# Optimization experiments

Hardware: AMD Instinct MI355X
Metric: run time of the kernel (lower is better)

Reference implementation:

```python
import jax, jax.numpy as jnp
import numpy as np

N = 4096
INPLANES = 256
PLANES = 256
LOC_PLANES = 256


def _ln(x, g, b, eps=1e-5):
    m = jnp.mean(x, axis=-1, keepdims=True)
    v = jnp.mean(jnp.square(x - m), axis=-1, keepdims=True)
    return (x - m) * jax.lax.rsqrt(v + eps) * g + b


def setup_inputs() -> dict:
    key = jax.random.key(0)
    ks = jax.random.split(key, 12)
    s = 0.02
    cat_dim = INPLANES + LOC_PLANES
    return {
        "img_fea": jax.random.normal(ks[0], (N, INPLANES), jnp.float32),
        "loc_fea": jax.random.normal(ks[1], (N, LOC_PLANES), jnp.float32),
        # conv11: Basic1d(cat_dim -> inplanes, bias=True) + ReLU
        "w11": jax.random.normal(ks[2], (cat_dim, INPLANES), jnp.float32) * s,
        "b11": jnp.zeros((INPLANES,), jnp.float32),
        # conv12: Linear(inplanes -> inplanes)
        "w12": jax.random.normal(ks[3], (INPLANES, INPLANES), jnp.float32) * s,
        "b12": jnp.zeros((INPLANES,), jnp.float32),
        # conv21: Basic1d(cat_dim -> inplanes, bias=True) + ReLU
        "w21": jax.random.normal(ks[4], (cat_dim, INPLANES), jnp.float32) * s,
        "b21": jnp.zeros((INPLANES,), jnp.float32),
        # conv22: Linear(inplanes -> inplanes*planes) -- hypernetwork weight generator
        "w22": jax.random.normal(ks[5], (INPLANES, INPLANES * PLANES), jnp.float32) * s,
        "b22": jnp.zeros((INPLANES * PLANES,), jnp.float32),
        # br: LayerNorm(planes)
        "lnbr_g": jnp.ones((PLANES,), jnp.float32),
        "lnbr_b": jnp.zeros((PLANES,), jnp.float32),
        # conv3: Basic1d(planes -> planes, bias=False) -> Linear + LayerNorm + ReLU
        "w3": jax.random.normal(ks[6], (PLANES, PLANES), jnp.float32) * s,
        "ln3_g": jnp.ones((PLANES,), jnp.float32),
        "ln3_b": jnp.zeros((PLANES,), jnp.float32),
    }


def reference(img_fea, loc_fea, w11, b11, w12, b12, w21, b21, w22, b22,
              lnbr_g, lnbr_b, w3, ln3_g, ln3_b):
    cat = jnp.concatenate([img_fea, loc_fea], axis=1)          # [N, 512]
    h11 = jax.nn.relu(cat @ w11 + b11)                          # [N, 256]
    wgt12 = h11 @ w12 + b12                                     # [N, 256]
    h21 = jax.nn.relu(cat @ w21 + b21)                          # [N, 256]
    wgt22 = (h21 @ w22 + b22).reshape(-1, INPLANES, PLANES)     # [N, 256, 256]
    out = jnp.einsum('bi,bio->bo', wgt12, wgt22)                # batched GEMV
    out = jax.nn.relu(_ln(out, lnbr_g, lnbr_b))
    out = jax.nn.relu(_ln(out @ w3, ln3_g, ln3_b))
    return (out, loc_fea)
```

## Files before the change

### kernel.cpp

```cpp
#include <hip/hip_runtime.h>
#include <stdint.h>

typedef unsigned short u16;
typedef __bf16 bf16;
typedef bf16 bf16x8 __attribute__((ext_vector_type(8)));
typedef u16 u16x8 __attribute__((ext_vector_type(8)));
typedef float f32x4 __attribute__((ext_vector_type(4)));

__device__ __forceinline__ u16 f2bf(float f) {
  union { float f; unsigned u; } v; v.f = f;
  unsigned u = v.u;
  u += 0x7FFFu + ((u >> 16) & 1u);
  return (u16)(u >> 16);
}

__device__ __forceinline__ bf16x8 as_bf16x8(u16x8 v) {
  return __builtin_bit_cast(bf16x8, v);
}

__device__ __forceinline__ f32x4 mfma16(bf16x8 a, bf16x8 b, f32x4 c) {
  return __builtin_amdgcn_mfma_f32_16x16x32_bf16(a, b, c, 0, 0, 0);
}

#define AS1 __attribute__((address_space(1)))
#define AS3 __attribute__((address_space(3)))
__device__ __forceinline__ void gl_lds16(const u16* g, u16* l) {
  __builtin_amdgcn_global_load_lds((const AS1 void*)g, (AS3 void*)l, 16, 0, 0);
}

__device__ __forceinline__ long wfrag(int b, int i) {
  const int bt = b >> 7, bg = (b >> 6) & 1, nf = (b >> 4) & 3, l15 = b & 15;
  const int ih = (i >> 7) & 1, s4 = (i >> 6) & 1, ks = (i >> 5) & 1;
  const int lhi = (i >> 3) & 3, e = i & 7;
  return ((((((((long)bt * 2 + ih) * 2 + bg) * 2 + s4) * 2 + ks) * 4 + lhi) * 4
            + nf) * 16 + l15) * 8 + e;
}

__global__ __launch_bounds__(256) void k_transpose(const float* __restrict__ src,
    u16* __restrict__ dst, long dstStride, long dstOff) {
  __shared__ float tile[64][65];
  const int t = threadIdx.x;
  const int tr = t >> 6, tc = t & 63;
  const long rb = (long)blockIdx.x * 64;
  const int ob = blockIdx.y * 64;
#pragma unroll
  for (int i = 0; i < 16; ++i) {
    int r = i * 4 + tr;
    tile[r][tc] = src[(rb + r) * 256 + ob + tc];
  }
  __syncthreads();
  const int orow = t >> 2, seg = t & 3;
#pragma unroll
  for (int h = 0; h < 2; ++h) {
    u16x8 v;
#pragma unroll
    for (int j = 0; j < 8; ++j) v[j] = f2bf(tile[seg * 16 + h * 8 + j][orow]);
    *(u16x8*)&dst[(long)(ob + orow) * dstStride + dstOff + rb + seg * 16 + h * 8] = v;
  }
}

__global__ __launch_bounds__(256) void k_transpose_multi(
    const float* __restrict__ b22, const float* __restrict__ w11,
    const float* __restrict__ w21, const float* __restrict__ w12,
    const float* __restrict__ w3, u16* __restrict__ W2T, u16* __restrict__ W11T,
    u16* __restrict__ W21T, u16* __restrict__ W12T, u16* __restrict__ W3T) {
  __shared__ float tile[64][65];
  const int x = blockIdx.x;
  const float* src; u16* dst; long stride, off; int rb;
  if (x < 4)       { src = b22; dst = W2T;  stride = 65792; off = 65536; rb = x; }
  else if (x < 12) { src = w11; dst = W11T; stride = 512;   off = 0;     rb = x - 4; }
  else if (x < 20) { src = w21; dst = W21T; stride = 512;   off = 0;     rb = x - 12; }
  else if (x < 24) { src = w12; dst = W12T; stride = 256;   off = 0;     rb = x - 20; }
  else             { src = w3;  dst = W3T;  stride = 256;   off = 0;     rb = x - 24; }
  const long rbase = (long)rb * 64;
  const int t = threadIdx.x;
  const int tr = t >> 6, tc = t & 63;
  const int ob = blockIdx.y * 64;
#pragma unroll
  for (int i = 0; i < 16; ++i) {
    int r = i * 4 + tr;
    tile[r][tc] = src[(rbase + r) * 256 + ob + tc];
  }
  __syncthreads();
  const int orow = t >> 2, seg = t & 3;
#pragma unroll
  for (int h = 0; h < 2; ++h) {
    u16x8 v;
#pragma unroll
    for (int j = 0; j < 8; ++j) v[j] = f2bf(tile[seg * 16 + h * 8 + j][orow]);
    *(u16x8*)&dst[(long)(ob + orow) * stride + off + rbase + seg * 16 + h * 8] = v;
  }
}

__device__ __forceinline__ void gemm_small_core(const float* A0, const float* A1,
    int K, const u16* WT, f32x4 (&acc)[4], int o0, long row) {
  const int lane = threadIdx.x & 63;
  const int l15 = lane & 15, lhi = lane >> 4;
  const int kg = lhi * 8;
  for (int ks = 0; ks < K; ks += 32) {
    int k = ks + kg;
    const float* ap = (A1 != nullptr && k >= 256) ? (A1 + row * 256 + (k - 256))
                                                  : (A0 + row * 256 + k);
    f32x4 f0 = *(const f32x4*)ap;
    f32x4 f1 = *(const f32x4*)(ap + 4);
    u16x8 a;
    a[0]=f2bf(f0[0]); a[1]=f2bf(f0[1]); a[2]=f2bf(f0[2]); a[3]=f2bf(f0[3]);
    a[4]=f2bf(f1[0]); a[5]=f2bf(f1[1]); a[6]=f2bf(f1[2]); a[7]=f2bf(f1[3]);
    bf16x8 av = as_bf16x8(a);
#pragma unroll
    for (int nf = 0; nf < 4; ++nf) {
      int o = o0 + nf * 16 + l15;
      u16x8 braw = *(const u16x8*)(WT + (long)o * K + k);
      acc[nf] = mfma16(av, as_bf16x8(braw), acc[nf]);
    }
  }
}

__global__ __launch_bounds__(256) void k_gemm_h21(const float* __restrict__ img,
    const float* __restrict__ loc, const u16* __restrict__ W21T,
    const float* __restrict__ b21, float* __restrict__ h21) {
  const int t = threadIdx.x;
  const int wid = t >> 6, lane = t & 63;
  const int l15 = lane & 15, lhi = lane >> 4;
  const int b0 = blockIdx.x * 16;
  const int o0 = wid * 64;
  const long row = b0 + l15;
  f32x4 acc[4] = {};
  gemm_small_core(img, loc, 512, W21T, acc, o0, row);
#pragma unroll
  for (int nf = 0; nf < 4; ++nf) {
    int o = o0 + nf * 16 + l15;
    float bs = b21[o];
#pragma unroll
    for (int r = 0; r < 4; ++r) {
      long b = b0 + lhi * 4 + r;
      h21[b * 256 + o] = fmaxf(acc[nf][r] + bs, 0.f);
    }
  }
}

__global__ __launch_bounds__(256) void k_fuse12(const float* __restrict__ img,
    const float* __restrict__ loc, const u16* __restrict__ W11T,
    const float* __restrict__ b11, const u16* __restrict__ W12T,
    const float* __restrict__ b12, u16* __restrict__ wgt12F) {
  __shared__ u16 A16[16][264];
  const int t = threadIdx.x;
  const int wid = t >> 6, lane = t & 63;
  const int l15 = lane & 15, lhi = lane >> 4;
  const int b0 = blockIdx.x * 16;
  const int o0 = wid * 64;
  const long row = b0 + l15;
  f32x4 a1[4] = {};
  gemm_small_core(img, loc, 512, W11T, a1, o0, row);
#pragma unroll
  for (int nf = 0; nf < 4; ++nf) {
    int o = o0 + nf * 16 + l15;
    float bs = b11[o];
#pragma unroll
    for (int r = 0; r < 4; ++r)
      A16[lhi * 4 + r][o] = f2bf(fmaxf(a1[nf][r] + bs, 0.f));
  }
  __syncthreads();
  f32x4 a2[4] = {};
  for (int ks = 0; ks < 256; ks += 32) {
    const int k = ks + lhi * 8;
    bf16x8 av = as_bf16x8(*(const u16x8*)&A16[l15][k]);
#pragma unroll
    for (int nf = 0; nf < 4; ++nf) {
      int o = o0 + nf * 16 + l15;
      u16x8 braw = *(const u16x8*)(W12T + (long)o * 256 + k);
      a2[nf] = mfma16(av, as_bf16x8(braw), a2[nf]);
    }
  }
#pragma unroll
  for (int nf = 0; nf < 4; ++nf) {
    const int i = o0 + nf * 16 + l15;
    const float bs = b12[i];
#pragma unroll
    for (int r = 0; r < 4; ++r) {
      const int b = b0 + lhi * 4 + r;
      wgt12F[wfrag(b, i)] = f2bf(a2[nf][r] + bs);
    }
  }
}

__global__ __launch_bounds__(256, 2) void k_big(const u16* __restrict__ W2T,
    const float* __restrict__ h21, const u16* __restrict__ wgt12F,
    float* __restrict__ partials) {
  __shared__ u16 ldsWh[16384];
  __shared__ u16 ldsA[2][8192];
  const int t = threadIdx.x;
  const int wid = t >> 6, lane = t & 63;
  const int l15 = lane & 15, lhi = lane >> 4;
  const int n = blockIdx.x;
  const int chunk = n & 7;
  const int q = n >> 3;
  const int o_base = (q & 1) * 128;
  const int bt = q >> 1;
  const int b0 = bt * 128;
  const int og = wid >> 1, bg = wid & 1;
  const int nkb = (chunk == 7) ? 33 : 32;
  const int NSh = nkb * 2;

  const int ar = t >> 1;
  const int ah = t & 1;
  const u16* agbase = W2T + (long)(o_base + ar) * 65792 + chunk * 8192 + ah * 32;

  f32x4 acc[4][4] = {};
  u16x8 sa[4];

  auto LOADA = [&](int poff) {
    const u16* p = agbase + poff;
#pragma unroll
    for (int j = 0; j < 4; ++j) sa[j] = *(const u16x8*)(p + j * 8);
  };
  auto WRITEA = [&](int buf) {
#pragma unroll
    for (int j = 0; j < 4; ++j) {
      const int sg = ah * 4 + j;
      *(u16x8*)&ldsA[buf][ar * 64 + ((sg ^ (ar & 7)) * 8)] = sa[j];
    }
  };

  const int bvb = (bg * 2048 + lhi * 128 + l15 * 2) * 4;

#pragma unroll 1
  for (int ih = 0; ih < 2; ++ih) {
    {
      const u16* wsrc = wgt12F + ((long)(bt * 2 + ih)) * 16384 + lane * 8;
#pragma unroll
      for (int j = 0; j < 8; ++j)
        gl_lds16(wsrc + (wid * 8 + j) * 512, &ldsWh[(wid * 8 + j) * 512]);
    }
    LOADA(ih * 128);
    WRITEA(0);
    __syncthreads();

    int s = 0;
#pragma unroll 1
    for (int kb = 0; kb < nkb; ++kb) {
      const int kk = chunk * 32 + kb;
      float sc[4];
#pragma unroll
      for (int nf = 0; nf < 4; ++nf)
        sc[nf] = (kk < 256)
                   ? h21[(long)(b0 + bg * 64 + nf * 16 + l15) * 256 + kk]
                   : 1.0f;
      f32x4 sub[4][4] = {};
#pragma unroll
      for (int s4 = 0; s4 < 2; ++s4) {
        const int buf = s & 1;
        const bool last = (s + 1 >= NSh);
        if (!last)
          LOADA(s4 == 0 ? kb * 256 + ih * 128 + 64 : (kb + 1) * 256 + ih * 128);
#pragma unroll
        for (int ks = 0; ks < 2; ++ks) {
          const int x = ks * 4 + lhi;
          bf16x8 af[4], bv[4];
#pragma unroll
          for (int mf = 0; mf < 4; ++mf) {
            const int ro = og * 64 + mf * 16 + l15;
            af[mf] = as_bf16x8(
                *(const u16x8*)&ldsA[buf][ro * 64 + ((x ^ (ro & 7)) * 8)]);
          }
          const int bvo = bvb + (s4 * 2 + ks) * 2048;
#pragma unroll
          for (int nf = 0; nf < 4; ++nf)
            bv[nf] = as_bf16x8(*(const u16x8*)&ldsWh[bvo + nf * 128]);
          __builtin_amdgcn_s_setprio(1);
#pragma unroll
          for (int mf = 0; mf < 4; ++mf)
#pragma unroll
            for (int nf = 0; nf < 4; ++nf)
              sub[mf][nf] = mfma16(af[mf], bv[nf], sub[mf][nf]);
          __builtin_amdgcn_s_setprio(0);
        }
        if (!last) WRITEA(buf ^ 1);
        __syncthreads();
        ++s;
      }
#pragma unroll
      for (int mf = 0; mf < 4; ++mf)
#pragma unroll
        for (int nf = 0; nf < 4; ++nf)
          acc[mf][nf] += sc[nf] * sub[mf][nf];
    }
  }

  const long cb = (long)chunk * (256L * 4096);
#pragma unroll
  for (int mf = 0; mf < 4; ++mf)
#pragma unroll
    for (int nf = 0; nf < 4; ++nf)
#pragma unroll
      for (int r = 0; r < 4; ++r) {
        const int o = o_base + og * 64 + mf * 16 + lhi * 4 + r;
        const int bgl = b0 + bg * 64 + nf * 16 + l15;
        partials[cb + (long)o * 4096 + bgl] = acc[mf][nf][r];
      }
}

__global__ __launch_bounds__(256) void k_tail(const float* __restrict__ parts,
    const float* __restrict__ lng, const float* __restrict__ lnb,
    const u16* __restrict__ W3T, const float* __restrict__ g3,
    const float* __restrict__ bb3, float* __restrict__ out) {
  __shared__ float tile[16][260];
  __shared__ u16 A16[16][264];
  __shared__ float s1s[4][16], s2s[4][16];
  __shared__ float mz[16], rz[16];
  const int t = threadIdx.x;
  const int b0 = blockIdx.x * 16;
  {
    const int oq = t >> 2, bseg = t & 3;
#pragma unroll
    for (int j = 0; j < 4; ++j) {
      const int o = oq + j * 64;
      f32x4 s = {};
#pragma unroll
      for (int c = 0; c < 8; ++c)
        s += *(const f32x4*)&parts[(long)c * (256L * 4096) + (long)o * 4096 + b0 + bseg * 4];
#pragma unroll
      for (int q = 0; q < 4; ++q) tile[bseg * 4 + q][o] = s[q];
    }
  }
  __syncthreads();
  {
    const int r = t >> 4, og = t & 15;
    float v[16];
    float s1 = 0.f, s2 = 0.f;
#pragma unroll
    for (int q = 0; q < 16; ++q) {
      float x = tile[r][og * 16 + q];
      v[q] = x; s1 += x; s2 += x * x;
    }
    s1 += __shfl_xor(s1, 1); s2 += __shfl_xor(s2, 1);
    s1 += __shfl_xor(s1, 2); s2 += __shfl_xor(s2, 2);
    s1 += __shfl_xor(s1, 4); s2 += __shfl_xor(s2, 4);
    s1 += __shfl_xor(s1, 8); s2 += __shfl_xor(s2, 8);
    float mean = s1 * (1.f / 256.f);
    float var = s2 * (1.f / 256.f) - mean * mean;
    float rstd = rsqrtf(var + 1e-5f);
    u16x8 w0, w1;
#pragma unroll
    for (int q = 0; q < 16; ++q) {
      int o = og * 16 + q;
      float x = (v[q] - mean) * rstd * lng[o] + lnb[o];
      x = fmaxf(x, 0.f);
      if (q < 8) w0[q] = f2bf(x); else w1[q - 8] = f2bf(x);
    }
    *(u16x8*)&A16[r][og * 16] = w0;
    *(u16x8*)&A16[r][og * 16 + 8] = w1;
  }
  __syncthreads();
  const int wid = t >> 6, lane = t & 63;
  const int l15 = lane & 15, lhi = lane >> 4;
  const int wo = wid * 64;
  f32x4 acc[4] = {};
  for (int ks = 0; ks < 256; ks += 32) {
    const int k = ks + lhi * 8;
    bf16x8 av = as_bf16x8(*(const u16x8*)&A16[l15][k]);
#pragma unroll
    for (int nf = 0; nf < 4; ++nf) {
      int o = wo + nf * 16 + l15;
      u16x8 braw = *(const u16x8*)(W3T + (long)o * 256 + k);
      acc[nf] = mfma16(av, as_bf16x8(braw), acc[nf]);
    }
  }
#pragma unroll
  for (int r = 0; r < 4; ++r) {
    float s1 = 0.f, s2 = 0.f;
#pragma unroll
    for (int nf = 0; nf < 4; ++nf) { float x = acc[nf][r]; s1 += x; s2 += x * x; }
    s1 += __shfl_xor(s1, 1); s2 += __shfl_xor(s2, 1);
    s1 += __shfl_xor(s1, 2); s2 += __shfl_xor(s2, 2);
    s1 += __shfl_xor(s1, 4); s2 += __shfl_xor(s2, 4);
    s1 += __shfl_xor(s1, 8); s2 += __shfl_xor(s2, 8);
    if (l15 == 0) { s1s[wid][lhi * 4 + r] = s1; s2s[wid][lhi * 4 + r] = s2; }
  }
  __syncthreads();
  if (t < 16) {
    float s1 = s1s[0][t] + s1s[1][t] + s1s[2][t] + s1s[3][t];
    float s2 = s2s[0][t] + s2s[1][t] + s2s[2][t] + s2s[3][t];
    float mean = s1 * (1.f / 256.f);
    float var = s2 * (1.f / 256.f) - mean * mean;
    mz[t] = mean; rz[t] = rsqrtf(var + 1e-5f);
  }
  __syncthreads();
#pragma unroll
  for (int r = 0; r < 4; ++r) {
    const int b = lhi * 4 + r;
    const float mean = mz[b], rstd = rz[b];
#pragma unroll
    for (int nf = 0; nf < 4; ++nf) {
      int o = wo + nf * 16 + l15;
      float x = (acc[nf][r] - mean) * rstd * g3[o] + bb3[o];
      out[(long)(b0 + b) * 256 + o] = fmaxf(x, 0.f);
    }
  }
}

extern "C" void kernel_launch(void* const* d_in, const int* in_sizes, int n_in,
                              void* d_out, int out_size, void* d_ws, size_t ws_size,
                              hipStream_t stream) {
  const float* img = (const float*)d_in[0];
  const float* loc = (const float*)d_in[1];
  const float* w11 = (const float*)d_in[2];
  const float* b11 = (const float*)d_in[3];
  const float* w12 = (const float*)d_in[4];
  const float* b12 = (const float*)d_in[5];
  const float* w21 = (const float*)d_in[6];
  const float* b21 = (const float*)d_in[7];
  const float* w22 = (const float*)d_in[8];
  const float* b22 = (const float*)d_in[9];
  const float* lng = (const float*)d_in[10];
  const float* lnb = (const float*)d_in[11];
  const float* w3  = (const float*)d_in[12];
  const float* g3  = (const float*)d_in[13];
  const float* bb3 = (const float*)d_in[14];

  char* ws = (char*)d_ws;
  u16* W2T    = (u16*)(ws);
  u16* W11T   = (u16*)(ws + 33685504);
  u16* W21T   = (u16*)(ws + 33947648);
  u16* W12T   = (u16*)(ws + 34209792);
  u16* W3T    = (u16*)(ws + 34340864);
  float* h21  = (float*)(ws + 38666240);
  u16* wgt12F = (u16*)(ws + 42860544);
  float* parts = (float*)(ws + 47054848);
  float* outp  = (float*)d_out;

  hipMemcpyAsync(outp + 1048576, loc, 4194304, hipMemcpyDeviceToDevice, stream);

  hipLaunchKernelGGL(k_transpose, dim3(1024, 4), dim3(256), 0, stream,
                     w22, W2T, (long)65792, (long)0);
  hipLaunchKernelGGL(k_transpose_multi, dim3(28, 4), dim3(256), 0, stream,
                     b22, w11, w21, w12, w3, W2T, W11T, W21T, W12T, W3T);

  hipLaunchKernelGGL(k_gemm_h21, dim3(256), dim3(256), 0, stream,
                     img, loc, W21T, b21, h21);
  hipLaunchKernelGGL(k_fuse12, dim3(256), dim3(256), 0, stream,
                     img, loc, W11T, b11, W12T, b12, wgt12F);

  hipLaunchKernelGGL(k_big, dim3(512), dim3(256), 0, stream,
                     W2T, h21, wgt12F, parts);

  hipLaunchKernelGGL(k_tail, dim3(256), dim3(256), 0, stream,
                     parts, lng, lnb, W3T, g3, bb3, outp);
}
```

Measured before the change: 326.8 us.

## Merge transpose and front GEMM launches; deepen global-to-LDS prefetch in main kernel

Folds the two weight transpose kernels into one launch and the h21 GEMM and fused conv11/conv12 kernel into one two-slice grid. This cuts launch overhead and lets independent blocks share the GPU. In the main batched kernel the A-tile register staging becomes two alternating register sets, so global loads are issued two stages ahead and the LDS write happens before compute. The aim is to hide global latency better, at the cost of more registers. The bvb offset is also re-expressed in different units.

```diff
diff --git a/kernel.cpp b/kernel.cpp
--- a/kernel.cpp
+++ b/kernel.cpp
@@ -36,43 +36,25 @@
             + nf) * 16 + l15) * 8 + e;
 }
 
-__global__ __launch_bounds__(256) void k_transpose(const float* __restrict__ src,
-    u16* __restrict__ dst, long dstStride, long dstOff) {
-  __shared__ float tile[64][65];
-  const int t = threadIdx.x;
-  const int tr = t >> 6, tc = t & 63;
-  const long rb = (long)blockIdx.x * 64;
-  const int ob = blockIdx.y * 64;
-#pragma unroll
-  for (int i = 0; i < 16; ++i) {
-    int r = i * 4 + tr;
-    tile[r][tc] = src[(rb + r) * 256 + ob + tc];
-  }
-  __syncthreads();
-  const int orow = t >> 2, seg = t & 3;
-#pragma unroll
-  for (int h = 0; h < 2; ++h) {
-    u16x8 v;
-#pragma unroll
-    for (int j = 0; j < 8; ++j) v[j] = f2bf(tile[seg * 16 + h * 8 + j][orow]);
-    *(u16x8*)&dst[(long)(ob + orow) * dstStride + dstOff + rb + seg * 16 + h * 8] = v;
-  }
-}
-
-__global__ __launch_bounds__(256) void k_transpose_multi(
-    const float* __restrict__ b22, const float* __restrict__ w11,
-    const float* __restrict__ w21, const float* __restrict__ w12,
-    const float* __restrict__ w3, u16* __restrict__ W2T, u16* __restrict__ W11T,
-    u16* __restrict__ W21T, u16* __restrict__ W12T, u16* __restrict__ W3T) {
+__global__ __launch_bounds__(256) void k_transpose_all(
+    const float* __restrict__ w22, const float* __restrict__ b22,
+    const float* __restrict__ w11, const float* __restrict__ w21,
+    const float* __restrict__ w12, const float* __restrict__ w3,
+    u16* __restrict__ W2T, u16* __restrict__ W11T, u16* __restrict__ W21T,
+    u16* __restrict__ W12T, u16* __restrict__ W3T) {
   __shared__ float tile[64][65];
   const int x = blockIdx.x;
-  const float* src; u16* dst; long stride, off; int rb;
-  if (x < 4)       { src = b22; dst = W2T;  stride = 65792; off = 65536; rb = x; }
-  else if (x < 12) { src = w11; dst = W11T; stride = 512;   off = 0;     rb = x - 4; }
-  else if (x < 20) { src = w21; dst = W21T; stride = 512;   off = 0;     rb = x - 12; }
-  else if (x < 24) { src = w12; dst = W12T; stride = 256;   off = 0;     rb = x - 20; }
-  else             { src = w3;  dst = W3T;  stride = 256;   off = 0;     rb = x - 24; }
-  const long rbase = (long)rb * 64;
+  const float* src; u16* dst; long stride, off; long rbase;
+  if (x < 1024)     { src = w22; dst = W2T;  stride = 65792; off = 0;
+                      rbase = (long)x * 64; }
+  else {
+    const int x2 = x - 1024;
+    if (x2 < 4)       { src = b22; dst = W2T;  stride = 65792; off = 65536; rbase = (long)x2 * 64; }
+    else if (x2 < 12) { src = w11; dst = W11T; stride = 512;   off = 0;     rbase = (long)(x2 - 4) * 64; }
+    else if (x2 < 20) { src = w21; dst = W21T; stride = 512;   off = 0;     rbase = (long)(x2 - 12) * 64; }
+    else if (x2 < 24) { src = w12; dst = W12T; stride = 256;   off = 0;     rbase = (long)(x2 - 20) * 64; }
+    else              { src = w3;  dst = W3T;  stride = 256;   off = 0;     rbase = (long)(x2 - 24) * 64; }
+  }
   const int t = threadIdx.x;
   const int tr = t >> 6, tc = t & 63;
   const int ob = blockIdx.y * 64;
@@ -116,33 +98,12 @@
   }
 }
 
-__global__ __launch_bounds__(256) void k_gemm_h21(const float* __restrict__ img,
-    const float* __restrict__ loc, const u16* __restrict__ W21T,
-    const float* __restrict__ b21, float* __restrict__ h21) {
-  const int t = threadIdx.x;
-  const int wid = t >> 6, lane = t & 63;
-  const int l15 = lane & 15, lhi = lane >> 4;
-  const int b0 = blockIdx.x * 16;
-  const int o0 = wid * 64;
-  const long row = b0 + l15;
-  f32x4 acc[4] = {};
-  gemm_small_core(img, loc, 512, W21T, acc, o0, row);
-#pragma unroll
-  for (int nf = 0; nf < 4; ++nf) {
-    int o = o0 + nf * 16 + l15;
-    float bs = b21[o];
-#pragma unroll
-    for (int r = 0; r < 4; ++r) {
-      long b = b0 + lhi * 4 + r;
-      h21[b * 256 + o] = fmaxf(acc[nf][r] + bs, 0.f);
-    }
-  }
-}
-
-__global__ __launch_bounds__(256) void k_fuse12(const float* __restrict__ img,
+__global__ __launch_bounds__(256) void k_front(const float* __restrict__ img,
     const float* __restrict__ loc, const u16* __restrict__ W11T,
     const float* __restrict__ b11, const u16* __restrict__ W12T,
-    const float* __restrict__ b12, u16* __restrict__ wgt12F) {
+    const float* __restrict__ b12, u16* __restrict__ wgt12F,
+    const u16* __restrict__ W21T, const float* __restrict__ b21,
+    float* __restrict__ h21) {
   __shared__ u16 A16[16][264];
   const int t = threadIdx.x;
   const int wid = t >> 6, lane = t & 63;
@@ -150,6 +111,21 @@
   const int b0 = blockIdx.x * 16;
   const int o0 = wid * 64;
   const long row = b0 + l15;
+  if (blockIdx.y == 1) {
+    f32x4 acc[4] = {};
+    gemm_small_core(img, loc, 512, W21T, acc, o0, row);
+#pragma unroll
+    for (int nf = 0; nf < 4; ++nf) {
+      int o = o0 + nf * 16 + l15;
+      float bs = b21[o];
+#pragma unroll
+      for (int r = 0; r < 4; ++r) {
+        long b = b0 + lhi * 4 + r;
+        h21[b * 256 + o] = fmaxf(acc[nf][r] + bs, 0.f);
+      }
+    }
+    return;
+  }
   f32x4 a1[4] = {};
   gemm_small_core(img, loc, 512, W11T, a1, o0, row);
 #pragma unroll
@@ -207,14 +183,14 @@
   const u16* agbase = W2T + (long)(o_base + ar) * 65792 + chunk * 8192 + ah * 32;
 
   f32x4 acc[4][4] = {};
-  u16x8 sa[4];
-
-  auto LOADA = [&](int poff) {
+  u16x8 saE[4], saO[4];
+
+  auto LOADA = [&](u16x8 (&sa)[4], int poff) {
     const u16* p = agbase + poff;
 #pragma unroll
     for (int j = 0; j < 4; ++j) sa[j] = *(const u16x8*)(p + j * 8);
   };
-  auto WRITEA = [&](int buf) {
+  auto WRITEA = [&](const u16x8 (&sa)[4], int buf) {
 #pragma unroll
     for (int j = 0; j < 4; ++j) {
       const int sg = ah * 4 + j;
@@ -222,21 +198,24 @@
     }
   };
 
-  const int bvb = (bg * 2048 + lhi * 128 + l15 * 2) * 4;
+  const int bvb = bg * 8192 + lhi * 512 + l15 * 8;
 
 #pragma unroll 1
   for (int ih = 0; ih < 2; ++ih) {
+    auto poff = [&](int s) {
+      return (s >> 1) * 256 + ih * 128 + (s & 1) * 64;
+    };
     {
       const u16* wsrc = wgt12F + ((long)(bt * 2 + ih)) * 16384 + lane * 8;
 #pragma unroll
       for (int j = 0; j < 8; ++j)
         gl_lds16(wsrc + (wid * 8 + j) * 512, &ldsWh[(wid * 8 + j) * 512]);
     }
-    LOADA(ih * 128);
-    WRITEA(0);
+    LOADA(saE, poff(0));
+    WRITEA(saE, 0);
+    LOADA(saO, poff(1));
     __syncthreads();
 
-    int s = 0;
 #pragma unroll 1
     for (int kb = 0; kb < nkb; ++kb) {
       const int kk = chunk * 32 + kb;
@@ -249,10 +228,14 @@
       f32x4 sub[4][4] = {};
 #pragma unroll
       for (int s4 = 0; s4 < 2; ++s4) {
-        const int buf = s & 1;
-        const bool last = (s + 1 >= NSh);
-        if (!last)
-          LOADA(s4 == 0 ? kb * 256 + ih * 128 + 64 : (kb + 1) * 256 + ih * 128);
+        const int s = kb * 2 + s4;
+        const int buf = s4;
+        if (s + 1 < NSh) {
+          if (s4 == 0) WRITEA(saO, 1); else WRITEA(saE, 0);
+        }
+        if (s + 2 < NSh) {
+          if (s4 == 0) LOADA(saE, poff(s + 2)); else LOADA(saO, poff(s + 2));
+        }
 #pragma unroll
         for (int ks = 0; ks < 2; ++ks) {
           const int x = ks * 4 + lhi;
@@ -275,9 +258,7 @@
               sub[mf][nf] = mfma16(af[mf], bv[nf], sub[mf][nf]);
           __builtin_amdgcn_s_setprio(0);
         }
-        if (!last) WRITEA(buf ^ 1);
         __syncthreads();
-        ++s;
       }
 #pragma unroll
       for (int mf = 0; mf < 4; ++mf)
@@ -431,15 +412,11 @@
 
   hipMemcpyAsync(outp + 1048576, loc, 4194304, hipMemcpyDeviceToDevice, stream);
 
-  hipLaunchKernelGGL(k_transpose, dim3(1024, 4), dim3(256), 0, stream,
-                     w22, W2T, (long)65792, (long)0);
-  hipLaunchKernelGGL(k_transpose_multi, dim3(28, 4), dim3(256), 0, stream,
-                     b22, w11, w21, w12, w3, W2T, W11T, W21T, W12T, W3T);
-
-  hipLaunchKernelGGL(k_gemm_h21, dim3(256), dim3(256), 0, stream,
-                     img, loc, W21T, b21, h21);
-  hipLaunchKernelGGL(k_fuse12, dim3(256), dim3(256), 0, stream,
-                     img, loc, W11T, b11, W12T, b12, wgt12F);
+  hipLaunchKernelGGL(k_transpose_all, dim3(1052, 4), dim3(256), 0, stream,
+                     w22, b22, w11, w21, w12, w3, W2T, W11T, W21T, W12T, W3T);
+
+  hipLaunchKernelGGL(k_front, dim3(256, 2), dim3(256), 0, stream,
+                     img, loc, W11T, b11, W12T, b12, wgt12F, W21T, b21, h21);
 
   hipLaunchKernelGGL(k_big, dim3(512), dim3(256), 0, stream,
                      W2T, h21, wgt12F, parts);
```

Measured after the change: 320.3 us. -2.0%, faster.
